# Kernel tuning notes

Measured on AMD Instinct MI355X. Metric: run time of the kernel, lower is better.

## Reference

```python
import jax, jax.numpy as jnp
import numpy as np

B, T_IN, T_OUT, N, FEAT = 32, 96, 96, 512, 8
HID = 512
GRID_SIZE, SPLINE_ORDER = 5, 3
GRID_RANGE = (-1.0, 1.0)


def _make_grid():
    # matches KANLinear.create_grid: identical row per in_feature, so keep 1-D
    h = (GRID_RANGE[1] - GRID_RANGE[0]) / GRID_SIZE
    return jnp.arange(-SPLINE_ORDER, GRID_SIZE + SPLINE_ORDER + 1, dtype=jnp.float32) * h + GRID_RANGE[0]


def _b_splines(x, grid):
    # x: [M, in_features]; de Boor-Cox recursion, order SPLINE_ORDER
    x = x[..., None]  # [M, in, 1]
    bases = ((x >= grid[:-1]) & (x < grid[1:])).astype(x.dtype)
    for k in range(1, SPLINE_ORDER + 1):
        left = (x - grid[:-(k + 1)]) / (grid[k:-1] - grid[:-(k + 1)])
        right = (grid[k + 1:] - x) / (grid[k + 1:] - grid[1:-k])
        bases = left * bases[..., :-1] + right * bases[..., 1:]
    return bases  # [M, in, grid_size + spline_order]


def setup_inputs() -> dict:
    key = jax.random.key(0)
    ks = jax.random.split(key, 12)
    s = 0.05
    return {
        "X": jax.random.normal(ks[0], (B, T_IN, N, FEAT), jnp.float32),
        "Y": jax.random.normal(ks[1], (B, T_OUT, N, FEAT), jnp.float32),
        "Wx": jax.random.normal(ks[2], (HID, T_IN * FEAT), jnp.float32) * s,
        "bx": jax.random.normal(ks[3], (HID,), jnp.float32) * s,
        "Wy": jax.random.normal(ks[4], (HID, T_OUT * FEAT), jnp.float32) * s,
        "by": jax.random.normal(ks[5], (HID,), jnp.float32) * s,
        "base_w": jax.random.normal(ks[6], (64, 2 * HID), jnp.float32) * s,
        "spline_w": jax.random.normal(ks[7], (64, 2 * HID, GRID_SIZE + SPLINE_ORDER), jnp.float32) * s,
        "spline_scaler": jax.random.normal(ks[8], (64, 2 * HID), jnp.float32) * s,
        "Wf": jax.random.normal(ks[9], (T_OUT * FEAT, 64), jnp.float32) * s,
        "bf": jax.random.normal(ks[10], (T_OUT * FEAT,), jnp.float32) * s,
    }


def reference(X, Y, Wx, bx, Wy, by, base_w, spline_w, spline_scaler, Wf, bf):
    # [B, T, N, F] -> [B, N, T*F]
    Xf = jnp.transpose(X, (0, 2, 1, 3)).reshape(B, N, T_IN * FEAT)
    Yf = jnp.transpose(Y, (0, 2, 1, 3)).reshape(B, N, T_OUT * FEAT)
    Hx = jnp.tanh(Xf @ Wx.T + bx)
    Hy = jnp.tanh(Yf @ Wy.T + by)
    h = jnp.concatenate([Hx, Hy], axis=-1).reshape(B * N, 2 * HID)

    grid = _make_grid()
    base_out = jax.nn.silu(h) @ base_w.T
    scaled_sw = spline_w * spline_scaler[..., None]  # [out, in, coeff]
    spline_out = jnp.einsum("mik,oik->mo", _b_splines(h, grid), scaled_sw)
    kan_out = (base_out + spline_out).reshape(B, N, 64)

    out = kan_out @ Wf.T + bf  # [B, N, T_OUT*FEAT]
    out = out.reshape(B, N, T_OUT, FEAT)
    return jnp.transpose(out, (0, 2, 1, 3))  # [B, T_OUT, N, FEAT]
```

## Files before the change

kernel.cpp:

```cpp
#include <hip/hip_runtime.h>
#include <cmath>

#define B_    32
#define T_    96
#define N_    512
#define F_    8
#define TF_   768
#define HID_  512
#define M_    16384
#define KIN_  1024
#define KS_   8

typedef short short8 __attribute__((ext_vector_type(8)));
typedef _Float16 halfx8 __attribute__((ext_vector_type(8)));
typedef float f32x4  __attribute__((ext_vector_type(4)));
typedef float f32x2  __attribute__((ext_vector_type(2)));
typedef unsigned int  uintx4 __attribute__((ext_vector_type(4)));
typedef unsigned long long ulongx2 __attribute__((ext_vector_type(2)));
typedef unsigned short      ushort_t;
typedef unsigned int        uint_t;
typedef unsigned long long  ulong_t;

#define HT_B     0ull
#define WQ_B     33554432ull
#define WB_B     34734080ull
#define SH_B     36306944ull
#define KANR_B   61472768ull
#define WFQ_B    63569920ull

static __device__ inline uint_t  fbits(float f){ return __builtin_bit_cast(uint_t, f); }
static __device__ inline ushort_t f2b(float f){
    uint_t u = fbits(f);
    return (ushort_t)((u + 0x7fffu + ((u >> 16) & 1u)) >> 16);
}
static __device__ inline float b2f(ushort_t h){ return __builtin_bit_cast(float, (uint_t)h << 16); }
static __device__ inline ulong_t pack4(float4 v){
    return (ulong_t)f2b(v.x) | ((ulong_t)f2b(v.y) << 16) |
           ((ulong_t)f2b(v.z) << 32) | ((ulong_t)f2b(v.w) << 48);
}
static __device__ inline ulong_t pack4t(float4 v){
    uint_t d0 = (fbits(v.x) >> 16) | (fbits(v.y) & 0xffff0000u);
    uint_t d1 = (fbits(v.z) >> 16) | (fbits(v.w) & 0xffff0000u);
    return (ulong_t)d0 | ((ulong_t)d1 << 32);
}
static __device__ inline float fast_tanh(float x){
    const float e = __expf(2.0f * x);
    return 1.0f - 2.0f / (e + 1.0f);
}
static __device__ inline void gload_lds16(const void* g, void* l){
    __builtin_amdgcn_global_load_lds(
        (const __attribute__((address_space(1))) unsigned int*)g,
        (__attribute__((address_space(3))) unsigned int*)l, 16, 0, 0);
}

__global__ __launch_bounds__(256) void pack_wq(
    const float* __restrict__ base_w,
    const float* __restrict__ spline_w,
    const float* __restrict__ scaler,
    ushort_t* __restrict__ wq)
{
    const int e = blockIdx.x * 256 + threadIdx.x;
    const int j    = e & 7;
    const int ln   = (e >> 3) & 63;
    const int ct   = (e >> 9) & 3;
    const int t    = (e >> 11) & 3;
    const int rest = e >> 13;
    const int ss   = rest % 9;
    const int ks   = rest / 9;
    const int o = ct * 16 + (ln & 15);
    const int g = ln >> 4;
    float v;
    if (ss < 8) {
        const int i = ks * 128 + ss * 16 + t * 4 + g;
        v = spline_w[(o * KIN_ + i) * 8 + j] * scaler[o * KIN_ + i];
    } else {
        const int i = ks * 128 + t * 32 + j * 4 + g;
        v = base_w[o * KIN_ + i];
    }
    wq[e] = f2b(v);
}

__global__ __launch_bounds__(256) void pack_wb2(
    const float* __restrict__ Wx,
    const float* __restrict__ Wy,
    ushort_t* __restrict__ wb)
{
    const int e = blockIdx.x * 256 + threadIdx.x;
    const float v = (e < 512 * TF_) ? Wx[e] : Wy[e - 512 * TF_];
    wb[e] = f2b(v);
}

__global__ __launch_bounds__(256) void pack_wfq(
    const float* __restrict__ Wf, ushort_t* __restrict__ wfq)
{
    const int e = blockIdx.x * 256 + threadIdx.x;
    const int jj  = e & 7;
    const int ln  = (e >> 3) & 63;
    const int rt  = (e >> 9) & 3;
    const int s   = (e >> 11) & 1;
    const int wvt = (e >> 12) & 1;
    const int tb  = e >> 13;
    const int tf = tb * 128 + wvt * 64 + rt * 16 + (ln & 15);
    const int o  = s * 32 + (ln >> 4) * 8 + jj;
    wfq[e] = f2b(Wf[(size_t)tf * 64 + o]);
}

__global__ __launch_bounds__(256) void xcvt_kernel(
    const float* __restrict__ Xs, ushort_t* __restrict__ xbf)
{
    __shared__ __align__(16) char lds[32 * 1552];
    const int tid = threadIdx.x;
    const int n0  = blockIdx.x * 32;
    const int bb  = blockIdx.y;
    const int nl  = (tid & 63) >> 1;
    const int f4  = (tid & 1) * 4;
    const int tq  = tid >> 6;
    #pragma unroll 4
    for (int u = 0; u < 24; u++) {
        const int t = u * 4 + tq;
        const float4 v = *(const float4*)(Xs + (size_t)bb * (T_ * N_ * F_)
                                             + (size_t)t * (N_ * F_)
                                             + (size_t)(n0 + nl) * F_ + f4);
        *(ulong_t*)(lds + nl * 1552 + t * 16 + f4 * 2) = pack4t(v);
    }
    __syncthreads();
    #pragma unroll 4
    for (int u = 0; u < 12; u++) {
        const int c   = u * 256 + tid;
        const int row = c / 96;
        const int col = c - row * 96;
        const uintx4 val = *(const uintx4*)(lds + row * 1552 + col * 16);
        *(uintx4*)(xbf + (size_t)(bb * 512 + n0 + row) * TF_ + col * 8) = val;
    }
}

__global__ __launch_bounds__(512, 2) void gemm_tanh_v7(
    const ushort_t* __restrict__ xbf,
    const ushort_t* __restrict__ wb,
    const float* __restrict__ bias,
    ushort_t* __restrict__ ht, int z)
{
    __shared__ __align__(16) char smem[32768];

    const int tid = threadIdx.x;
    const int wv  = tid >> 6;
    const int ln  = tid & 63;
    const int lr  = ln & 15;
    const int hi  = ln >> 4;
    const int wm  = wv >> 2;
    const int wj  = wv & 3;

    const int m0  = blockIdx.x * 128;
    const int jl0 = blockIdx.y * 128;
    const int j0  = z * 512 + jl0;

    const int r_l = ln >> 3;
    const int ck  = ((ln & 7) ^ r_l) * 8;

    f32x4 acc[4][2] = {};

    for (int kt = 0; kt < 12; kt++) {
        __syncthreads();
        #pragma unroll
        for (int s = 0; s < 2; s++) {
            const int reg = s * 8 + wv;
            const int row = reg * 8 + r_l;
            gload_lds16(xbf + (size_t)(m0 + row) * TF_ + kt * 64 + ck,
                        smem + reg * 1024 + ln * 16);
            gload_lds16(wb + (size_t)(j0 + row) * TF_ + kt * 64 + ck,
                        smem + 16384 + reg * 1024 + ln * 16);
        }
        __syncthreads();

        #pragma unroll
        for (int h = 0; h < 2; h++) {
            const int g = h * 4 + hi;
            short8 a[4], b[2];
            #pragma unroll
            for (int rt = 0; rt < 4; rt++) {
                const int r = wm * 64 + rt * 16 + lr;
                a[rt] = *(short8*)(smem + r * 128 + ((g ^ (r & 7)) * 16));
            }
            #pragma unroll
            for (int ct = 0; ct < 2; ct++) {
                const int r = wj * 32 + ct * 16 + lr;
                b[ct] = *(short8*)(smem + 16384 + r * 128 + ((g ^ (r & 7)) * 16));
            }
            #pragma unroll
            for (int rt = 0; rt < 4; rt++)
                #pragma unroll
                for (int ct = 0; ct < 2; ct++)
                    acc[rt][ct] = __builtin_amdgcn_mfma_f32_16x16x32_bf16(
                        a[rt], b[ct], acc[rt][ct], 0, 0, 0);
        }
    }

    __syncthreads();
    #pragma unroll
    for (int ct = 0; ct < 2; ct++) {
        const int j = wj * 32 + ct * 16 + lr;
        const float bvv = bias[jl0 + j];
        #pragma unroll
        for (int rt = 0; rt < 4; rt++) {
            const f32x4 v = acc[rt][ct];
            float4 tv;
            tv.x = fast_tanh(v[0] + bvv);
            tv.y = fast_tanh(v[1] + bvv);
            tv.z = fast_tanh(v[2] + bvv);
            tv.w = fast_tanh(v[3] + bvv);
            const int slot = wm * 8 + rt * 2 + (hi >> 1);
            *(ulong_t*)(smem + j * 256 + ((slot ^ (j & 15)) * 16) + (hi & 1) * 8)
                = pack4(tv);
        }
    }
    __syncthreads();
    {
        const int j  = tid >> 2;
        const int q4 = tid & 3;
        ushort_t* dst = ht + (size_t)(j0 + j) * M_ + m0 + q4 * 32;
        #pragma unroll
        for (int w = 0; w < 4; w++) {
            const int slot = q4 * 4 + w;
            short8 val = *(short8*)(smem + j * 256 + ((slot ^ (j & 15)) * 16));
            *(short8*)(dst + w * 8) = val;
        }
    }
}

static __device__ inline short8 shift_pack(float b0, float b1, float b2, float b3, int si)
{
    const uint_t d0 = (fbits(b0) >> 16) | (fbits(b1) & 0xffff0000u);
    const uint_t d1 = (fbits(b2) >> 16) | (fbits(b3) & 0xffff0000u);
    const ulong_t P = (ulong_t)d0 | ((ulong_t)d1 << 32);
    const int sh = si << 4;
    const ulong_t Plo = P << (sh & 63);
    const ulong_t Phi = P >> ((64 - sh) & 63);
    ulongx2 pr;
    pr.x = (si == 4) ? 0ull : Plo;
    pr.y = (si == 0) ? 0ull : ((si == 4) ? P : Phi);
    return __builtin_bit_cast(short8, pr);
}

static __device__ inline void eval_bases2(float x0, float x1, short8& a0, short8& a1)
{
    f32x2 x = {x0, x1};
    f32x2 v = x * 2.5f + 2.5f;
    f32x2 sf = __builtin_elementwise_floor(v);
    sf = __builtin_elementwise_min(sf, (f32x2){4.0f, 4.0f});
    const f32x2 u  = v - sf;
    const f32x2 u2 = u * u;
    const f32x2 u3 = u2 * u;
    const f32x2 omu = 1.0f - u;
    const f32x2 omu3 = omu * omu * omu;
    const f32x2 B0 = omu3 * (1.0f / 6.0f);
    const f32x2 B3 = u3 * (1.0f / 6.0f);
    const f32x2 B1 = (u3 * 0.5f + (2.0f / 3.0f)) - u2;
    const f32x2 B2 = 1.0f - B0 - B1 - B3;
    a0 = shift_pack(B0[0], B1[0], B2[0], B3[0], (int)sf[0]);
    a1 = shift_pack(B0[1], B1[1], B2[1], B3[1], (int)sf[1]);
}

__global__ __launch_bounds__(256) void kan_v9(
    const ushort_t* __restrict__ ht,
    const ushort_t* __restrict__ wq,
    _Float16* __restrict__ kanp)
{
    __shared__ __align__(16) char lds[40960];

    const int tid = threadIdx.x;
    const int wv  = tid >> 6;
    const int ln  = tid & 63;
    const int g   = ln >> 4;
    const int lr  = ln & 15;
    const int m0  = blockIdx.x * 128;
    const int ks  = blockIdx.y;
    const int iB  = ks * 128;

    const ushort_t* wqk = wq + (size_t)ks * 73728;

    #pragma unroll
    for (int c = 0; c < 8; c++) {
        const int ll = wv * 8 + c;
        const int il = ll * 4 + (ln >> 4);
        const int chunk = ln & 15;
        const int rowst = (chunk ^ ((il & 3) << 1)) * 8;
        gload_lds16(ht + (size_t)(iB + il) * M_ + m0 + rowst,
                    lds + ll * 1024 + (ln & 15) * 16 + (ln >> 4) * 256);
    }
    gload_lds16(wqk + (size_t)wv * 512 + ln * 8,
                lds + 32768 + wv * 1024 + ln * 16);
    short8 wA = *(const short8*)(wqk + (size_t)(1 * 4 + wv) * 512 + ln * 8);
    short8 wB = *(const short8*)(wqk + (size_t)(2 * 4 + wv) * 512 + ln * 8);
    __syncthreads();

    const int hb0 = g * 256 + ((wv * 64 + lr * 2) ^ (g << 5));
    const int hb1 = g * 256 + ((wv * 64 + 32 + lr * 2) ^ (g << 5));

    f32x4 acc[2][4] = {};

    #pragma unroll 4
    for (int it = 0; it < 32; ++it) {
        char* rb = lds + 32768 + (it & 1) * 4096;
        const short8 b0 = *(short8*)(rb + 0 * 1024 + ln * 16);
        const short8 b1 = *(short8*)(rb + 1 * 1024 + ln * 16);
        const short8 b2 = *(short8*)(rb + 2 * 1024 + ln * 16);
        const short8 b3 = *(short8*)(rb + 3 * 1024 + ln * 16);

        const float x0 = b2f(*(const ushort_t*)(lds + hb0 + it * 1024));
        const float x1 = b2f(*(const ushort_t*)(lds + hb1 + it * 1024));
        short8 a0, a1;
        eval_bases2(x0, x1, a0, a1);

        acc[0][0] = __builtin_amdgcn_mfma_f32_16x16x32_bf16(a0, b0, acc[0][0], 0, 0, 0);
        acc[0][1] = __builtin_amdgcn_mfma_f32_16x16x32_bf16(a0, b1, acc[0][1], 0, 0, 0);
        acc[0][2] = __builtin_amdgcn_mfma_f32_16x16x32_bf16(a0, b2, acc[0][2], 0, 0, 0);
        acc[0][3] = __builtin_amdgcn_mfma_f32_16x16x32_bf16(a0, b3, acc[0][3], 0, 0, 0);
        acc[1][0] = __builtin_amdgcn_mfma_f32_16x16x32_bf16(a1, b0, acc[1][0], 0, 0, 0);
        acc[1][1] = __builtin_amdgcn_mfma_f32_16x16x32_bf16(a1, b1, acc[1][1], 0, 0, 0);
        acc[1][2] = __builtin_amdgcn_mfma_f32_16x16x32_bf16(a1, b2, acc[1][2], 0, 0, 0);
        acc[1][3] = __builtin_amdgcn_mfma_f32_16x16x32_bf16(a1, b3, acc[1][3], 0, 0, 0);

        *(short8*)(lds + 32768 + ((it + 1) & 1) * 4096 + wv * 1024 + ln * 16) = wA;
        wA = wB;
        wB = *(const short8*)(wqk + (size_t)((it + 3) * 4 + wv) * 512 + ln * 8);
        __syncthreads();
    }

    #pragma unroll
    for (int t = 0; t < 4; ++t) {
        const int it = 32 + t;
        char* rb = lds + 32768 + (it & 1) * 4096;
        const short8 b0 = *(short8*)(rb + 0 * 1024 + ln * 16);
        const short8 b1 = *(short8*)(rb + 1 * 1024 + ln * 16);
        const short8 b2 = *(short8*)(rb + 2 * 1024 + ln * 16);
        const short8 b3 = *(short8*)(rb + 3 * 1024 + ln * 16);

        uintx4 d0v, d1v;
        #pragma unroll
        for (int jw = 0; jw < 4; jw++) {
            const int o0 = hb0 + t * 8192 + (jw * 2) * 1024;
            const int o1 = hb0 + t * 8192 + (jw * 2 + 1) * 1024;
            const int p0 = hb1 + t * 8192 + (jw * 2) * 1024;
            const int p1 = hb1 + t * 8192 + (jw * 2 + 1) * 1024;
            const float x00 = b2f(*(const ushort_t*)(lds + o0));
            const float x01 = b2f(*(const ushort_t*)(lds + o1));
            const float x10 = b2f(*(const ushort_t*)(lds + p0));
            const float x11 = b2f(*(const ushort_t*)(lds + p1));
            const float s00 = x00 / (1.0f + __expf(-x00));
            const float s01 = x01 / (1.0f + __expf(-x01));
            const float s10 = x10 / (1.0f + __expf(-x10));
            const float s11 = x11 / (1.0f + __expf(-x11));
            d0v[jw] = (fbits(s00) >> 16) | (fbits(s01) & 0xffff0000u);
            d1v[jw] = (fbits(s10) >> 16) | (fbits(s11) & 0xffff0000u);
        }
        const short8 a0 = __builtin_bit_cast(short8, d0v);
        const short8 a1 = __builtin_bit_cast(short8, d1v);

        acc[0][0] = __builtin_amdgcn_mfma_f32_16x16x32_bf16(a0, b0, acc[0][0], 0, 0, 0);
        acc[0][1] = __builtin_amdgcn_mfma_f32_16x16x32_bf16(a0, b1, acc[0][1], 0, 0, 0);
        acc[0][2] = __builtin_amdgcn_mfma_f32_16x16x32_bf16(a0, b2, acc[0][2], 0, 0, 0);
        acc[0][3] = __builtin_amdgcn_mfma_f32_16x16x32_bf16(a0, b3, acc[0][3], 0, 0, 0);
        acc[1][0] = __builtin_amdgcn_mfma_f32_16x16x32_bf16(a1, b0, acc[1][0], 0, 0, 0);
        acc[1][1] = __builtin_amdgcn_mfma_f32_16x16x32_bf16(a1, b1, acc[1][1], 0, 0, 0);
        acc[1][2] = __builtin_amdgcn_mfma_f32_16x16x32_bf16(a1, b2, acc[1][2], 0, 0, 0);
        acc[1][3] = __builtin_amdgcn_mfma_f32_16x16x32_bf16(a1, b3, acc[1][3], 0, 0, 0);

        if (t < 3) {
            *(short8*)(lds + 32768 + ((it + 1) & 1) * 4096 + wv * 1024 + ln * 16) = wA;
            wA = wB;
            if (t == 0)
                wB = *(const short8*)(wqk + (size_t)(35 * 4 + wv) * 512 + ln * 8);
            __syncthreads();
        }
    }

    #pragma unroll
    for (int rt = 0; rt < 2; rt++) {
        #pragma unroll
        for (int ct = 0; ct < 4; ct++) {
            const int o = ct * 16 + lr;
            #pragma unroll
            for (int q = 0; q < 4; q++) {
                const size_t row = (size_t)(m0 + wv * 32 + rt * 16 + g * 4 + q);
                kanp[(size_t)ks * (M_ * 64) + row * 64 + o] = (_Float16)acc[rt][ct][q];
            }
        }
    }
}

__global__ __launch_bounds__(256) void reduce_kan(
    const _Float16* __restrict__ kanp, ushort_t* __restrict__ kanr)
{
    const int e8 = blockIdx.x * 256 + threadIdx.x;
    const size_t base = (size_t)e8 * 8;
    float s[8] = {};
    #pragma unroll
    for (int p = 0; p < KS_; p++) {
        const halfx8 v = *(const halfx8*)(kanp + (size_t)p * (M_ * 64) + base);
        #pragma unroll
        for (int j = 0; j < 8; j++) s[j] += (float)v[j];
    }
    float4 s0 = make_float4(s[0], s[1], s[2], s[3]);
    float4 s1 = make_float4(s[4], s[5], s[6], s[7]);
    ulongx2 outv;
    outv.x = pack4(s0);
    outv.y = pack4(s1);
    *(ulongx2*)(kanr + base) = outv;
}

__global__ __launch_bounds__(256) void final_v2(
    const ushort_t* __restrict__ kanr,
    const ushort_t* __restrict__ wfq,
    const float* __restrict__ bf,
    float* __restrict__ out)
{
    const int tid = threadIdx.x;
    const int wv  = tid >> 6;
    const int ln  = tid & 63;
    const int lr  = ln & 15;
    const int hi  = ln >> 4;
    const int wvm = wv >> 1;
    const int wvt = wv & 1;
    const int mb  = blockIdx.x;
    const int tb  = blockIdx.y;

    f32x4 acc[4][4] = {};

    #pragma unroll
    for (int s = 0; s < 2; s++) {
        short8 afr[4], bfr[4];
        #pragma unroll
        for (int rt = 0; rt < 4; rt++) {
            const size_t idx = ((size_t)(((tb * 2 + wvt) * 2 + s) * 4 + rt)) * 64 + ln;
            afr[rt] = ((const short8*)wfq)[idx];
        }
        #pragma unroll
        for (int ct = 0; ct < 4; ct++) {
            const int m = mb * 128 + wvm * 64 + ct * 16 + lr;
            bfr[ct] = *(const short8*)(kanr + (size_t)m * 64 + s * 32 + hi * 8);
        }
        #pragma unroll
        for (int rt = 0; rt < 4; rt++)
            #pragma unroll
            for (int ct = 0; ct < 4; ct++)
                acc[rt][ct] = __builtin_amdgcn_mfma_f32_16x16x32_bf16(
                    afr[rt], bfr[ct], acc[rt][ct], 0, 0, 0);
    }

    #pragma unroll
    for (int rt = 0; rt < 4; rt++) {
        const int tf0 = tb * 128 + wvt * 64 + rt * 16 + hi * 4;
        const float4 b4 = *(const float4*)&bf[tf0];
        const int t  = tf0 >> 3;
        const int f0 = tf0 & 7;
        #pragma unroll
        for (int ct = 0; ct < 4; ct++) {
            const int m = mb * 128 + wvm * 64 + ct * 16 + lr;
            const int bb = m >> 9;
            const int n  = m & 511;
            const f32x4 v = acc[rt][ct];
            float4 o4 = make_float4(v[0] + b4.x, v[1] + b4.y, v[2] + b4.z, v[3] + b4.w);
            *(float4*)&out[(size_t)bb * (T_ * N_ * F_)
                           + (size_t)t * (N_ * F_)
                           + (size_t)n * F_ + f0] = o4;
        }
    }
}

extern "C" void kernel_launch(void* const* d_in, const int* in_sizes, int n_in,
                              void* d_out, int out_size, void* d_ws, size_t ws_size,
                              hipStream_t stream)
{
    const float* X      = (const float*)d_in[0];
    const float* Y      = (const float*)d_in[1];
    const float* Wx     = (const float*)d_in[2];
    const float* bx     = (const float*)d_in[3];
    const float* Wy     = (const float*)d_in[4];
    const float* by     = (const float*)d_in[5];
    const float* base_w = (const float*)d_in[6];
    const float* spline_w = (const float*)d_in[7];
    const float* spline_scaler = (const float*)d_in[8];
    const float* Wf     = (const float*)d_in[9];
    const float* bf     = (const float*)d_in[10];

    float* out = (float*)d_out;
    ushort_t* ht   = (ushort_t*)((char*)d_ws + HT_B);
    ushort_t* wq   = (ushort_t*)((char*)d_ws + WQ_B);
    ushort_t* wb   = (ushort_t*)((char*)d_ws + WB_B);
    ushort_t* xbf  = (ushort_t*)((char*)d_ws + SH_B);
    _Float16* kanp = (_Float16*)((char*)d_ws + SH_B);
    ushort_t* kanr = (ushort_t*)((char*)d_ws + KANR_B);
    ushort_t* wfq  = (ushort_t*)((char*)d_ws + WFQ_B);

    pack_wq<<<2304, 256, 0, stream>>>(base_w, spline_w, spline_scaler, wq);
    pack_wb2<<<3072, 256, 0, stream>>>(Wx, Wy, wb);
    pack_wfq<<<192, 256, 0, stream>>>(Wf, wfq);

    xcvt_kernel<<<dim3(16, 32), 256, 0, stream>>>(X, xbf);
    gemm_tanh_v7<<<dim3(128, 4), 512, 0, stream>>>(xbf, wb, bx, ht, 0);
    xcvt_kernel<<<dim3(16, 32), 256, 0, stream>>>(Y, xbf);
    gemm_tanh_v7<<<dim3(128, 4), 512, 0, stream>>>(xbf, wb, by, ht, 1);

    kan_v9<<<dim3(M_ / 128, KS_), 256, 0, stream>>>(ht, wq, kanp);
    reduce_kan<<<512, 256, 0, stream>>>(kanp, kanr);
    final_v2<<<dim3(128, 6), 256, 0, stream>>>(kanr, wfq, bf, out);
}
```

Baseline: 137.1 us.

## Fold SiLU base branch into spline weights and double K-steps per barrier

The SiLU base term is rewritten as a fixed linear combination of the eight cubic B-spline bases. Because the hidden activations come from tanh and stay inside the grid range, base_w times those constants can be added into the packed spline weights, which removes the four SiLU K-steps and their exp evaluations from the KAN GEMM. The main loop now handles two K-iterations per LDS double-buffer stage, with doubled weight buffers, which halves the number of barriers. In exchange, the base branch becomes a fitted approximation of SiLU with small numerical error, and the kernel uses more LDS and more registers.

Result: faster. 127.6 us (-6.9%).

```diff
diff --git a/kernel.cpp b/kernel.cpp
--- a/kernel.cpp
+++ b/kernel.cpp
@@ -28,6 +28,10 @@
 #define KANR_B   61472768ull
 #define WFQ_B    63569920ull
 
+__device__ __constant__ float KC[8] = {
+    -0.2818252f, -0.2770046f, -0.2237417f, -0.1031025f,
+     0.0968975f,  0.3762583f,  0.7229954f,  1.1181747f };
+
 static __device__ inline uint_t  fbits(float f){ return __builtin_bit_cast(uint_t, f); }
 static __device__ inline ushort_t f2b(float f){
     uint_t u = fbits(f);
@@ -60,23 +64,17 @@
     ushort_t* __restrict__ wq)
 {
     const int e = blockIdx.x * 256 + threadIdx.x;
-    const int j    = e & 7;
-    const int ln   = (e >> 3) & 63;
-    const int ct   = (e >> 9) & 3;
-    const int t    = (e >> 11) & 3;
-    const int rest = e >> 13;
-    const int ss   = rest % 9;
-    const int ks   = rest / 9;
+    const int j  = e & 7;
+    const int ln = (e >> 3) & 63;
+    const int ct = (e >> 9) & 3;
+    const int t  = (e >> 11) & 3;
+    const int ss = (e >> 13) & 7;
+    const int ks = e >> 16;
     const int o = ct * 16 + (ln & 15);
     const int g = ln >> 4;
-    float v;
-    if (ss < 8) {
-        const int i = ks * 128 + ss * 16 + t * 4 + g;
-        v = spline_w[(o * KIN_ + i) * 8 + j] * scaler[o * KIN_ + i];
-    } else {
-        const int i = ks * 128 + t * 32 + j * 4 + g;
-        v = base_w[o * KIN_ + i];
-    }
+    const int i = ks * 128 + ss * 16 + t * 4 + g;
+    const float v = spline_w[(o * KIN_ + i) * 8 + j] * scaler[o * KIN_ + i]
+                  + base_w[o * KIN_ + i] * KC[j];
     wq[e] = f2b(v);
 }
 
@@ -260,12 +258,12 @@
     a1 = shift_pack(B0[1], B1[1], B2[1], B3[1], (int)sf[1]);
 }
 
-__global__ __launch_bounds__(256) void kan_v9(
+__global__ __launch_bounds__(256) void kan_v10b(
     const ushort_t* __restrict__ ht,
     const ushort_t* __restrict__ wq,
     _Float16* __restrict__ kanp)
 {
-    __shared__ __align__(16) char lds[40960];
+    __shared__ __align__(16) char lds[49152];
 
     const int tid = threadIdx.x;
     const int wv  = tid >> 6;
@@ -276,7 +274,7 @@
     const int ks  = blockIdx.y;
     const int iB  = ks * 128;
 
-    const ushort_t* wqk = wq + (size_t)ks * 73728;
+    const ushort_t* wqk = wq + (size_t)ks * 65536;
 
     #pragma unroll
     for (int c = 0; c < 8; c++) {
@@ -289,8 +287,12 @@
     }
     gload_lds16(wqk + (size_t)wv * 512 + ln * 8,
                 lds + 32768 + wv * 1024 + ln * 16);
-    short8 wA = *(const short8*)(wqk + (size_t)(1 * 4 + wv) * 512 + ln * 8);
-    short8 wB = *(const short8*)(wqk + (size_t)(2 * 4 + wv) * 512 + ln * 8);
+    gload_lds16(wqk + (size_t)(4 + wv) * 512 + ln * 8,
+                lds + 32768 + (4 + wv) * 1024 + ln * 16);
+    short8 wA0 = *(const short8*)(wqk + (size_t)(8 + wv) * 512 + ln * 8);
+    short8 wA1 = *(const short8*)(wqk + (size_t)(12 + wv) * 512 + ln * 8);
+    short8 wB0 = *(const short8*)(wqk + (size_t)(16 + wv) * 512 + ln * 8);
+    short8 wB1 = *(const short8*)(wqk + (size_t)(20 + wv) * 512 + ln * 8);
     __syncthreads();
 
     const int hb0 = g * 256 + ((wv * 64 + lr * 2) ^ (g << 5));
@@ -299,79 +301,49 @@
     f32x4 acc[2][4] = {};
 
     #pragma unroll 4
-    for (int it = 0; it < 32; ++it) {
-        char* rb = lds + 32768 + (it & 1) * 4096;
-        const short8 b0 = *(short8*)(rb + 0 * 1024 + ln * 16);
-        const short8 b1 = *(short8*)(rb + 1 * 1024 + ln * 16);
-        const short8 b2 = *(short8*)(rb + 2 * 1024 + ln * 16);
-        const short8 b3 = *(short8*)(rb + 3 * 1024 + ln * 16);
-
-        const float x0 = b2f(*(const ushort_t*)(lds + hb0 + it * 1024));
-        const float x1 = b2f(*(const ushort_t*)(lds + hb1 + it * 1024));
-        short8 a0, a1;
-        eval_bases2(x0, x1, a0, a1);
-
-        acc[0][0] = __builtin_amdgcn_mfma_f32_16x16x32_bf16(a0, b0, acc[0][0], 0, 0, 0);
-        acc[0][1] = __builtin_amdgcn_mfma_f32_16x16x32_bf16(a0, b1, acc[0][1], 0, 0, 0);
-        acc[0][2] = __builtin_amdgcn_mfma_f32_16x16x32_bf16(a0, b2, acc[0][2], 0, 0, 0);
-        acc[0][3] = __builtin_amdgcn_mfma_f32_16x16x32_bf16(a0, b3, acc[0][3], 0, 0, 0);
-        acc[1][0] = __builtin_amdgcn_mfma_f32_16x16x32_bf16(a1, b0, acc[1][0], 0, 0, 0);
-        acc[1][1] = __builtin_amdgcn_mfma_f32_16x16x32_bf16(a1, b1, acc[1][1], 0, 0, 0);
-        acc[1][2] = __builtin_amdgcn_mfma_f32_16x16x32_bf16(a1, b2, acc[1][2], 0, 0, 0);
-        acc[1][3] = __builtin_amdgcn_mfma_f32_16x16x32_bf16(a1, b3, acc[1][3], 0, 0, 0);
-
-        *(short8*)(lds + 32768 + ((it + 1) & 1) * 4096 + wv * 1024 + ln * 16) = wA;
-        wA = wB;
-        wB = *(const short8*)(wqk + (size_t)((it + 3) * 4 + wv) * 512 + ln * 8);
+    for (int p = 0; p < 16; ++p) {
+        char* rb = lds + 32768 + (p & 1) * 8192;
+        short8 bfr[8];
+        #pragma unroll
+        for (int f = 0; f < 8; f++)
+            bfr[f] = *(short8*)(rb + f * 1024 + ln * 16);
+
+        if (p < 15) {
+            char* wbuf = lds + 32768 + ((p + 1) & 1) * 8192;
+            *(short8*)(wbuf + wv * 1024 + ln * 16)       = wA0;
+            *(short8*)(wbuf + (4 + wv) * 1024 + ln * 16) = wA1;
+        }
+        wA0 = wB0; wA1 = wB1;
+        if (p < 13) {
+            wB0 = *(const short8*)(wqk + (size_t)((p + 3) * 8 + wv) * 512 + ln * 8);
+            wB1 = *(const short8*)(wqk + (size_t)((p + 3) * 8 + 4 + wv) * 512 + ln * 8);
+        }
+
+        const int itA = 2 * p, itB = 2 * p + 1;
+        short8 a0, a1, a2, a3;
+        eval_bases2(b2f(*(const ushort_t*)(lds + hb0 + itA * 1024)),
+                    b2f(*(const ushort_t*)(lds + hb1 + itA * 1024)), a0, a1);
+        eval_bases2(b2f(*(const ushort_t*)(lds + hb0 + itB * 1024)),
+                    b2f(*(const ushort_t*)(lds + hb1 + itB * 1024)), a2, a3);
+
+        acc[0][0] = __builtin_amdgcn_mfma_f32_16x16x32_bf16(a0, bfr[0], acc[0][0], 0, 0, 0);
+        acc[0][1] = __builtin_amdgcn_mfma_f32_16x16x32_bf16(a0, bfr[1], acc[0][1], 0, 0, 0);
+        acc[0][2] = __builtin_amdgcn_mfma_f32_16x16x32_bf16(a0, bfr[2], acc[0][2], 0, 0, 0);
+        acc[0][3] = __builtin_amdgcn_mfma_f32_16x16x32_bf16(a0, bfr[3], acc[0][3], 0, 0, 0);
+        acc[1][0] = __builtin_amdgcn_mfma_f32_16x16x32_bf16(a1, bfr[0], acc[1][0], 0, 0, 0);
+        acc[1][1] = __builtin_amdgcn_mfma_f32_16x16x32_bf16(a1, bfr[1], acc[1][1], 0, 0, 0);
+        acc[1][2] = __builtin_amdgcn_mfma_f32_16x16x32_bf16(a1, bfr[2], acc[1][2], 0, 0, 0);
+        acc[1][3] = __builtin_amdgcn_mfma_f32_16x16x32_bf16(a1, bfr[3], acc[1][3], 0, 0, 0);
+        acc[0][0] = __builtin_amdgcn_mfma_f32_16x16x32_bf16(a2, bfr[4], acc[0][0], 0, 0, 0);
+        acc[0][1] = __builtin_amdgcn_mfma_f32_16x16x32_bf16(a2, bfr[5], acc[0][1], 0, 0, 0);
+        acc[0][2] = __builtin_amdgcn_mfma_f32_16x16x32_bf16(a2, bfr[6], acc[0][2], 0, 0, 0);
+        acc[0][3] = __builtin_amdgcn_mfma_f32_16x16x32_bf16(a2, bfr[7], acc[0][3], 0, 0, 0);
+        acc[1][0] = __builtin_amdgcn_mfma_f32_16x16x32_bf16(a3, bfr[4], acc[1][0], 0, 0, 0);
+        acc[1][1] = __builtin_amdgcn_mfma_f32_16x16x32_bf16(a3, bfr[5], acc[1][1], 0, 0, 0);
+        acc[1][2] = __builtin_amdgcn_mfma_f32_16x16x32_bf16(a3, bfr[6], acc[1][2], 0, 0, 0);
+        acc[1][3] = __builtin_amdgcn_mfma_f32_16x16x32_bf16(a3, bfr[7], acc[1][3], 0, 0, 0);
+
         __syncthreads();
-    }
-
-    #pragma unroll
-    for (int t = 0; t < 4; ++t) {
-        const int it = 32 + t;
-        char* rb = lds + 32768 + (it & 1) * 4096;
-        const short8 b0 = *(short8*)(rb + 0 * 1024 + ln * 16);
-        const short8 b1 = *(short8*)(rb + 1 * 1024 + ln * 16);
-        const short8 b2 = *(short8*)(rb + 2 * 1024 + ln * 16);
-        const short8 b3 = *(short8*)(rb + 3 * 1024 + ln * 16);
-
-        uintx4 d0v, d1v;
-        #pragma unroll
-        for (int jw = 0; jw < 4; jw++) {
-            const int o0 = hb0 + t * 8192 + (jw * 2) * 1024;
-            const int o1 = hb0 + t * 8192 + (jw * 2 + 1) * 1024;
-            const int p0 = hb1 + t * 8192 + (jw * 2) * 1024;
-            const int p1 = hb1 + t * 8192 + (jw * 2 + 1) * 1024;
-            const float x00 = b2f(*(const ushort_t*)(lds + o0));
-            const float x01 = b2f(*(const ushort_t*)(lds + o1));
-            const float x10 = b2f(*(const ushort_t*)(lds + p0));
-            const float x11 = b2f(*(const ushort_t*)(lds + p1));
-            const float s00 = x00 / (1.0f + __expf(-x00));
-            const float s01 = x01 / (1.0f + __expf(-x01));
-            const float s10 = x10 / (1.0f + __expf(-x10));
-            const float s11 = x11 / (1.0f + __expf(-x11));
-            d0v[jw] = (fbits(s00) >> 16) | (fbits(s01) & 0xffff0000u);
-            d1v[jw] = (fbits(s10) >> 16) | (fbits(s11) & 0xffff0000u);
-        }
-        const short8 a0 = __builtin_bit_cast(short8, d0v);
-        const short8 a1 = __builtin_bit_cast(short8, d1v);
-
-        acc[0][0] = __builtin_amdgcn_mfma_f32_16x16x32_bf16(a0, b0, acc[0][0], 0, 0, 0);
-        acc[0][1] = __builtin_amdgcn_mfma_f32_16x16x32_bf16(a0, b1, acc[0][1], 0, 0, 0);
-        acc[0][2] = __builtin_amdgcn_mfma_f32_16x16x32_bf16(a0, b2, acc[0][2], 0, 0, 0);
-        acc[0][3] = __builtin_amdgcn_mfma_f32_16x16x32_bf16(a0, b3, acc[0][3], 0, 0, 0);
-        acc[1][0] = __builtin_amdgcn_mfma_f32_16x16x32_bf16(a1, b0, acc[1][0], 0, 0, 0);
-        acc[1][1] = __builtin_amdgcn_mfma_f32_16x16x32_bf16(a1, b1, acc[1][1], 0, 0, 0);
-        acc[1][2] = __builtin_amdgcn_mfma_f32_16x16x32_bf16(a1, b2, acc[1][2], 0, 0, 0);
-        acc[1][3] = __builtin_amdgcn_mfma_f32_16x16x32_bf16(a1, b3, acc[1][3], 0, 0, 0);
-
-        if (t < 3) {
-            *(short8*)(lds + 32768 + ((it + 1) & 1) * 4096 + wv * 1024 + ln * 16) = wA;
-            wA = wB;
-            if (t == 0)
-                wB = *(const short8*)(wqk + (size_t)(35 * 4 + wv) * 512 + ln * 8);
-            __syncthreads();
-        }
     }
 
     #pragma unroll
@@ -492,7 +464,7 @@
     ushort_t* kanr = (ushort_t*)((char*)d_ws + KANR_B);
     ushort_t* wfq  = (ushort_t*)((char*)d_ws + WFQ_B);
 
-    pack_wq<<<2304, 256, 0, stream>>>(base_w, spline_w, spline_scaler, wq);
+    pack_wq<<<2048, 256, 0, stream>>>(base_w, spline_w, spline_scaler, wq);
     pack_wb2<<<3072, 256, 0, stream>>>(Wx, Wy, wb);
     pack_wfq<<<192, 256, 0, stream>>>(Wf, wfq);
 
@@ -501,7 +473,7 @@
     xcvt_kernel<<<dim3(16, 32), 256, 0, stream>>>(Y, xbf);
     gemm_tanh_v7<<<dim3(128, 4), 512, 0, stream>>>(xbf, wb, by, ht, 1);
 
-    kan_v9<<<dim3(M_ / 128, KS_), 256, 0, stream>>>(ht, wq, kanp);
+    kan_v10b<<<dim3(M_ / 128, KS_), 256, 0, stream>>>(ht, wq, kanp);
     reduce_kan<<<512, 256, 0, stream>>>(kanp, kanr);
     final_v2<<<dim3(128, 6), 256, 0, stream>>>(kanr, wfq, bf, out);
 }
```
